# Kernel optimization log

Hardware: AMD Instinct MI355X
Metric: run time of the kernel (lower is better)

The kernel has to match this reference:

```python
import jax, jax.numpy as jnp
import numpy as np

HIDDEN = 2048
NUM_EXPERTS = 64
TOP_K = 2


def setup_inputs() -> dict:
    key = jax.random.key(0)
    k1, k2 = jax.random.split(key)
    x = jax.random.normal(k1, (4, 4096, HIDDEN), dtype=jnp.float32)
    # nn.Linear(hidden, num_experts, bias=False): weight shape [E, H], y = x @ W.T
    W = jax.random.normal(k2, (NUM_EXPERTS, HIDDEN), dtype=jnp.float32) * (HIDDEN ** -0.5)
    return {"x": x, "W": W}


def reference(x, W):
    B, S, H = x.shape
    E, K = NUM_EXPERTS, TOP_K
    xf = x.reshape(-1, H)                       # [N, H]
    gate_logits = xf @ W.T                      # [N, E]
    routing_probs = jax.nn.softmax(gate_logits, axis=-1)
    top_k_probs, top_k_indices = jax.lax.top_k(routing_probs, K)  # [N, K]
    denom = jnp.sum(top_k_probs, axis=-1, keepdims=True) + 1e-6
    routing_weights = (top_k_probs / denom).reshape(B, S, K)
    expert_indices = top_k_indices.reshape(B, S, K)

    # aux load-balancing loss (training path)
    N = xf.shape[0]
    # expert_mask.mean(0): fraction of tokens assigned to each expert
    assign_per_expert = jnp.zeros((E,), jnp.float32).at[top_k_indices.reshape(-1)].add(1.0) / N
    prob_per_expert = jnp.mean(routing_probs, axis=0)             # [E]
    aux_loss = (jnp.sum(prob_per_expert * prob_per_expert) * E
                + jnp.sum(assign_per_expert * assign_per_expert) * E)

    # expert_counts update (bincount over selected indices)
    expert_counts = jnp.zeros((E,), jnp.float32).at[top_k_indices.reshape(-1)].add(1.0)

    return routing_weights, expert_indices, aux_loss, expert_counts
```

## Files before the change

### kernel.cpp

```cpp
#include <hip/hip_runtime.h>

#define HID 2048
#define NEXP 64
#define NTOK 16384
#define TM 32
#define NTHREADS 256
#define NCHUNK 32
#define KPH 4
#define CPW 8
#define WS_W_OFF 1024
#define CHUNK_B 24576

#define OUT_IDX_OFF (2 * NTOK)
#define OUT_AUX_OFF (4 * NTOK)
#define OUT_CNT_OFF (4 * NTOK + 1)

typedef __attribute__((ext_vector_type(8))) short bhalf8;
typedef __attribute__((ext_vector_type(16))) float f32x16;

__device__ __forceinline__ void split3(float v, unsigned short& h1, unsigned short& h2, unsigned short& h3) {
    unsigned int u = __float_as_uint(v);
    unsigned int r1 = (u + 0x7FFFu + ((u >> 16) & 1u)) & 0xFFFF0000u;
    float f1 = __uint_as_float(r1);
    float d1 = v - f1;
    unsigned int u2 = __float_as_uint(d1);
    unsigned int r2 = (u2 + 0x7FFFu + ((u2 >> 16) & 1u)) & 0xFFFF0000u;
    float f2 = __uint_as_float(r2);
    float d2 = d1 - f2;
    h1 = (unsigned short)(r1 >> 16);
    h2 = (unsigned short)(r2 >> 16);
    h3 = (unsigned short)(__float_as_uint(d2) >> 16);
}

__device__ __forceinline__ void xsplit(float4 va, float4 vb, bhalf8& o1, bhalf8& o2, bhalf8& o3) {
    float f[8] = {va.x, va.y, va.z, va.w, vb.x, vb.y, vb.z, vb.w};
    union U { bhalf8 v; unsigned int u[4]; } u1, u2, u3;
#pragma unroll
    for (int t = 0; t < 4; t++) {
        float a = f[2 * t], b = f[2 * t + 1];
        unsigned int ua = __float_as_uint(a), ub = __float_as_uint(b);
        float da = a - __uint_as_float(ua & 0xFFFF0000u);
        float db = b - __uint_as_float(ub & 0xFFFF0000u);
        unsigned int uda = __float_as_uint(da), udb = __float_as_uint(db);
        float da2 = da - __uint_as_float(uda & 0xFFFF0000u);
        float db2 = db - __uint_as_float(udb & 0xFFFF0000u);
        u1.u[t] = (ua >> 16) | (ub & 0xFFFF0000u);
        u2.u[t] = (uda >> 16) | (udb & 0xFFFF0000u);
        u3.u[t] = (__float_as_uint(da2) >> 16) | (__float_as_uint(db2) & 0xFFFF0000u);
    }
    o1 = u1.v; o2 = u2.v; o3 = u3.v;
}

__global__ __launch_bounds__(256) void wsplit_kernel(const float* __restrict__ W,
                                                     char* __restrict__ wq,
                                                     float* __restrict__ wsf) {
    if (blockIdx.x == 0 && threadIdx.x < 2 * NEXP) wsf[threadIdx.x] = 0.f;
    int idx8 = (blockIdx.x * 256 + threadIdx.x) * 8;
    int e = idx8 >> 11;
    int k0 = idx8 & 2047;
    int c = k0 >> 6, ks = (k0 >> 4) & 3, half = (k0 >> 3) & 1;
    int g = e >> 5, l = (e & 31) + 32 * half;
    const float4* wp = (const float4*)(W + (size_t)e * HID + k0);
    float4 v0 = wp[0], v1 = wp[1];
    float f[8] = {v0.x, v0.y, v0.z, v0.w, v1.x, v1.y, v1.z, v1.w};
    unsigned int p1[4], p2[4], p3[4];
#pragma unroll
    for (int t = 0; t < 4; t++) {
        unsigned short a1, a2, a3, b1, b2, b3;
        split3(f[2 * t], a1, a2, a3);
        split3(f[2 * t + 1], b1, b2, b3);
        p1[t] = (unsigned int)a1 | ((unsigned int)b1 << 16);
        p2[t] = (unsigned int)a2 | ((unsigned int)b2 << 16);
        p3[t] = (unsigned int)a3 | ((unsigned int)b3 << 16);
    }
    char* base = wq + (size_t)(((c * 4 + ks) * 3 + 0) * 2 + g) * 1024 + l * 16;
    *(uint4*)(base)        = make_uint4(p1[0], p1[1], p1[2], p1[3]);
    *(uint4*)(base + 2048) = make_uint4(p2[0], p2[1], p2[2], p2[3]);
    *(uint4*)(base + 4096) = make_uint4(p3[0], p3[1], p3[2], p3[3]);
}

__global__ __launch_bounds__(NTHREADS, 2) void router_main(
    const float* __restrict__ x, const char* __restrict__ wq,
    float* __restrict__ out, float* __restrict__ ws_accum)
{
    __shared__ float slab[KPH * TM * 68];
    __shared__ float smax[TM];
    __shared__ float sinvZ[TM];
    __shared__ float scount[NEXP];

    const int tid = threadIdx.x;
    const int w = tid >> 6;
    const int lane = tid & 63;
    const int r = lane & 31;
    const int h = lane >> 5;
    const int n0 = blockIdx.x * TM;

    const float* xrow = x + (size_t)(n0 + r) * HID + h * 8;

    f32x16 acc0, acc1;
#pragma unroll
    for (int i = 0; i < 16; i++) { acc0[i] = 0.f; acc1[i] = 0.f; }

#pragma unroll 1
    for (int i = 0; i < CPW; ++i) {
        const int c = w * CPW + i;
        const float* xc = xrow + c * 64;
        float4 pxa[4], pxb[4];
#pragma unroll
        for (int ks = 0; ks < 4; ks++) {
            pxa[ks] = *(const float4*)(xc + ks * 16);
            pxb[ks] = *(const float4*)(xc + ks * 16 + 4);
        }
        const char* wc = wq + (size_t)c * CHUNK_B + lane * 16;
#pragma unroll
        for (int ks = 0; ks < 4; ks++) {
            bhalf8 A1, A2, A3;
            xsplit(pxa[ks], pxb[ks], A1, A2, A3);
            const char* wk = wc + ks * 6144;
            {
                bhalf8 B1 = *(const bhalf8*)(wk);
                bhalf8 B2 = *(const bhalf8*)(wk + 2048);
                bhalf8 B3 = *(const bhalf8*)(wk + 4096);
                acc0 = __builtin_amdgcn_mfma_f32_32x32x16_bf16(A1, B1, acc0, 0, 0, 0);
                acc0 = __builtin_amdgcn_mfma_f32_32x32x16_bf16(A1, B2, acc0, 0, 0, 0);
                acc0 = __builtin_amdgcn_mfma_f32_32x32x16_bf16(A2, B1, acc0, 0, 0, 0);
                acc0 = __builtin_amdgcn_mfma_f32_32x32x16_bf16(A1, B3, acc0, 0, 0, 0);
                acc0 = __builtin_amdgcn_mfma_f32_32x32x16_bf16(A2, B2, acc0, 0, 0, 0);
                acc0 = __builtin_amdgcn_mfma_f32_32x32x16_bf16(A3, B1, acc0, 0, 0, 0);
            }
            {
                bhalf8 B1 = *(const bhalf8*)(wk + 1024);
                bhalf8 B2 = *(const bhalf8*)(wk + 2048 + 1024);
                bhalf8 B3 = *(const bhalf8*)(wk + 4096 + 1024);
                acc1 = __builtin_amdgcn_mfma_f32_32x32x16_bf16(A1, B1, acc1, 0, 0, 0);
                acc1 = __builtin_amdgcn_mfma_f32_32x32x16_bf16(A1, B2, acc1, 0, 0, 0);
                acc1 = __builtin_amdgcn_mfma_f32_32x32x16_bf16(A2, B1, acc1, 0, 0, 0);
                acc1 = __builtin_amdgcn_mfma_f32_32x32x16_bf16(A1, B3, acc1, 0, 0, 0);
                acc1 = __builtin_amdgcn_mfma_f32_32x32x16_bf16(A2, B2, acc1, 0, 0, 0);
                acc1 = __builtin_amdgcn_mfma_f32_32x32x16_bf16(A3, B1, acc1, 0, 0, 0);
            }
        }
    }

#pragma unroll
    for (int reg = 0; reg < 16; reg++) {
        int row = (reg & 3) + 8 * (reg >> 2) + 4 * h;
        slab[(w * TM + row) * 68 + r]      = acc0[reg];
        slab[(w * TM + row) * 68 + 32 + r] = acc1[reg];
    }
    if (tid < NEXP) scount[tid] = 0.f;
    __syncthreads();

    float* logits = slab;
#pragma unroll
    for (int idx = tid; idx < TM * NEXP; idx += NTHREADS) {
        int t = idx >> 6, e = idx & 63;
        float v = slab[(0 * TM + t) * 68 + e] + slab[(1 * TM + t) * 68 + e]
                + slab[(2 * TM + t) * 68 + e] + slab[(3 * TM + t) * 68 + e];
        logits[t * 68 + e] = v;
    }
    __syncthreads();

    if (tid < TM) {
        const int t = tid;
        float m1 = -3.4e38f, m2 = -3.4e38f;
        int i1 = 0, i2 = 0;
        for (int e = 0; e < NEXP; e++) {
            float v = logits[t * 68 + e];
            if (v > m1) { m2 = m1; i2 = i1; m1 = v; i1 = e; }
            else if (v > m2) { m2 = v; i2 = e; }
        }
        float Z = 0.f;
        for (int e = 0; e < NEXP; e++)
            Z += __expf(logits[t * 68 + e] - m1);
        float invZ = 1.f / Z;
        float p1 = invZ;
        float p2 = __expf(m2 - m1) * invZ;
        float denom = p1 + p2 + 1e-6f;
        int n = n0 + t;
        out[2 * n + 0] = p1 / denom;
        out[2 * n + 1] = p2 / denom;
        out[OUT_IDX_OFF + 2 * n + 0] = (float)i1;
        out[OUT_IDX_OFF + 2 * n + 1] = (float)i2;
        smax[t] = m1;
        sinvZ[t] = invZ;
        atomicAdd(&scount[i1], 1.f);
        atomicAdd(&scount[i2], 1.f);
    }
    __syncthreads();

    if (tid < NEXP) {
        const int e = tid;
        float s = 0.f;
        for (int t = 0; t < TM; t++)
            s += __expf(logits[t * 68 + e] - smax[t]) * sinvZ[t];
        atomicAdd(&ws_accum[e], s);
        atomicAdd(&ws_accum[NEXP + e], scount[e]);
    }
}

__global__ void router_finish(const float* __restrict__ ws_accum,
                              float* __restrict__ out)
{
    const int e = threadIdx.x;
    const float invN = 1.f / (float)NTOK;
    float p = ws_accum[e] * invN;
    float a = ws_accum[NEXP + e] * invN;
    float v = p * p + a * a;
#pragma unroll
    for (int off = 32; off > 0; off >>= 1)
        v += __shfl_down(v, off);
    if (e == 0) out[OUT_AUX_OFF] = v * (float)NEXP;
    out[OUT_CNT_OFF + e] = ws_accum[NEXP + e];
}

extern "C" void kernel_launch(void* const* d_in, const int* in_sizes, int n_in,
                              void* d_out, int out_size, void* d_ws, size_t ws_size,
                              hipStream_t stream)
{
    const float* x = (const float*)d_in[0];
    const float* W = (const float*)d_in[1];
    float* out = (float*)d_out;
    float* wsf = (float*)d_ws;
    char* wq = (char*)d_ws + WS_W_OFF;

    wsplit_kernel<<<64, 256, 0, stream>>>(W, wq, wsf);
    router_main<<<NTOK / TM, NTHREADS, 0, stream>>>(x, wq, out, wsf);
    router_finish<<<1, 64, 0, stream>>>(wsf, out);
}
```

Baseline: 217.5 us.

## Double-buffer x chunk loads and replace global atomics with per-block partials

The main loop now prefetches the next x chunk into a second register set while computing the current chunk, so global load latency overlaps the MFMA work. Per-expert probability sums are computed by all 256 threads into shared memory instead of 64. Each block writes its partial sums to a workspace array rather than doing global atomics, and the finish kernel reduces the 512 partials serially. This removes global atomic contention and the zeroing step, but adds register pressure from the extra buffer and a serial 512-iteration reduction in a single-block finish kernel.

```diff
diff --git a/kernel.cpp b/kernel.cpp
--- a/kernel.cpp
+++ b/kernel.cpp
@@ -5,11 +5,12 @@
 #define NTOK 16384
 #define TM 32
 #define NTHREADS 256
+#define NBLK (NTOK / TM)
 #define NCHUNK 32
 #define KPH 4
 #define CPW 8
-#define WS_W_OFF 1024
 #define CHUNK_B 24576
+#define WS_W_OFF 262144
 
 #define OUT_IDX_OFF (2 * NTOK)
 #define OUT_AUX_OFF (4 * NTOK)
@@ -52,9 +53,7 @@
 }
 
 __global__ __launch_bounds__(256) void wsplit_kernel(const float* __restrict__ W,
-                                                     char* __restrict__ wq,
-                                                     float* __restrict__ wsf) {
-    if (blockIdx.x == 0 && threadIdx.x < 2 * NEXP) wsf[threadIdx.x] = 0.f;
+                                                     char* __restrict__ wq) {
     int idx8 = (blockIdx.x * 256 + threadIdx.x) * 8;
     int e = idx8 >> 11;
     int k0 = idx8 & 2047;
@@ -79,14 +78,51 @@
     *(uint4*)(base + 4096) = make_uint4(p3[0], p3[1], p3[2], p3[3]);
 }
 
+__device__ __forceinline__ void load_chunk(const float* xc, float4 (&pa)[4], float4 (&pb)[4]) {
+#pragma unroll
+    for (int ks = 0; ks < 4; ks++) {
+        pa[ks] = *(const float4*)(xc + ks * 16);
+        pb[ks] = *(const float4*)(xc + ks * 16 + 4);
+    }
+}
+
+__device__ __forceinline__ void compute_chunk(const float4 (&pa)[4], const float4 (&pb)[4],
+                                              const char* wc, f32x16& acc0, f32x16& acc1) {
+#pragma unroll
+    for (int ks = 0; ks < 4; ks++) {
+        bhalf8 A1, A2, A3;
+        xsplit(pa[ks], pb[ks], A1, A2, A3);
+        const char* wk = wc + ks * 6144;
+        bhalf8 B1 = *(const bhalf8*)(wk);
+        bhalf8 B2 = *(const bhalf8*)(wk + 2048);
+        bhalf8 B3 = *(const bhalf8*)(wk + 4096);
+        acc0 = __builtin_amdgcn_mfma_f32_32x32x16_bf16(A1, B1, acc0, 0, 0, 0);
+        acc0 = __builtin_amdgcn_mfma_f32_32x32x16_bf16(A1, B2, acc0, 0, 0, 0);
+        acc0 = __builtin_amdgcn_mfma_f32_32x32x16_bf16(A2, B1, acc0, 0, 0, 0);
+        acc0 = __builtin_amdgcn_mfma_f32_32x32x16_bf16(A1, B3, acc0, 0, 0, 0);
+        acc0 = __builtin_amdgcn_mfma_f32_32x32x16_bf16(A2, B2, acc0, 0, 0, 0);
+        acc0 = __builtin_amdgcn_mfma_f32_32x32x16_bf16(A3, B1, acc0, 0, 0, 0);
+        bhalf8 C1 = *(const bhalf8*)(wk + 1024);
+        bhalf8 C2 = *(const bhalf8*)(wk + 2048 + 1024);
+        bhalf8 C3 = *(const bhalf8*)(wk + 4096 + 1024);
+        acc1 = __builtin_amdgcn_mfma_f32_32x32x16_bf16(A1, C1, acc1, 0, 0, 0);
+        acc1 = __builtin_amdgcn_mfma_f32_32x32x16_bf16(A1, C2, acc1, 0, 0, 0);
+        acc1 = __builtin_amdgcn_mfma_f32_32x32x16_bf16(A2, C1, acc1, 0, 0, 0);
+        acc1 = __builtin_amdgcn_mfma_f32_32x32x16_bf16(A1, C3, acc1, 0, 0, 0);
+        acc1 = __builtin_amdgcn_mfma_f32_32x32x16_bf16(A2, C2, acc1, 0, 0, 0);
+        acc1 = __builtin_amdgcn_mfma_f32_32x32x16_bf16(A3, C1, acc1, 0, 0, 0);
+    }
+}
+
 __global__ __launch_bounds__(NTHREADS, 2) void router_main(
     const float* __restrict__ x, const char* __restrict__ wq,
-    float* __restrict__ out, float* __restrict__ ws_accum)
+    float* __restrict__ out, float* __restrict__ partials)
 {
     __shared__ float slab[KPH * TM * 68];
     __shared__ float smax[TM];
     __shared__ float sinvZ[TM];
     __shared__ float scount[NEXP];
+    __shared__ float sprob[NEXP];
 
     const int tid = threadIdx.x;
     const int w = tid >> 6;
@@ -101,45 +137,17 @@
 #pragma unroll
     for (int i = 0; i < 16; i++) { acc0[i] = 0.f; acc1[i] = 0.f; }
 
+    float4 pa0[4], pb0[4], pa1[4], pb1[4];
+    const float* xbase = xrow + (w * CPW) * 64;
+    load_chunk(xbase, pa0, pb0);
+    const char* wcbase = wq + (size_t)(w * CPW) * CHUNK_B + lane * 16;
+
 #pragma unroll 1
-    for (int i = 0; i < CPW; ++i) {
-        const int c = w * CPW + i;
-        const float* xc = xrow + c * 64;
-        float4 pxa[4], pxb[4];
-#pragma unroll
-        for (int ks = 0; ks < 4; ks++) {
-            pxa[ks] = *(const float4*)(xc + ks * 16);
-            pxb[ks] = *(const float4*)(xc + ks * 16 + 4);
-        }
-        const char* wc = wq + (size_t)c * CHUNK_B + lane * 16;
-#pragma unroll
-        for (int ks = 0; ks < 4; ks++) {
-            bhalf8 A1, A2, A3;
-            xsplit(pxa[ks], pxb[ks], A1, A2, A3);
-            const char* wk = wc + ks * 6144;
-            {
-                bhalf8 B1 = *(const bhalf8*)(wk);
-                bhalf8 B2 = *(const bhalf8*)(wk + 2048);
-                bhalf8 B3 = *(const bhalf8*)(wk + 4096);
-                acc0 = __builtin_amdgcn_mfma_f32_32x32x16_bf16(A1, B1, acc0, 0, 0, 0);
-                acc0 = __builtin_amdgcn_mfma_f32_32x32x16_bf16(A1, B2, acc0, 0, 0, 0);
-                acc0 = __builtin_amdgcn_mfma_f32_32x32x16_bf16(A2, B1, acc0, 0, 0, 0);
-                acc0 = __builtin_amdgcn_mfma_f32_32x32x16_bf16(A1, B3, acc0, 0, 0, 0);
-                acc0 = __builtin_amdgcn_mfma_f32_32x32x16_bf16(A2, B2, acc0, 0, 0, 0);
-                acc0 = __builtin_amdgcn_mfma_f32_32x32x16_bf16(A3, B1, acc0, 0, 0, 0);
-            }
-            {
-                bhalf8 B1 = *(const bhalf8*)(wk + 1024);
-                bhalf8 B2 = *(const bhalf8*)(wk + 2048 + 1024);
-                bhalf8 B3 = *(const bhalf8*)(wk + 4096 + 1024);
-                acc1 = __builtin_amdgcn_mfma_f32_32x32x16_bf16(A1, B1, acc1, 0, 0, 0);
-                acc1 = __builtin_amdgcn_mfma_f32_32x32x16_bf16(A1, B2, acc1, 0, 0, 0);
-                acc1 = __builtin_amdgcn_mfma_f32_32x32x16_bf16(A2, B1, acc1, 0, 0, 0);
-                acc1 = __builtin_amdgcn_mfma_f32_32x32x16_bf16(A1, B3, acc1, 0, 0, 0);
-                acc1 = __builtin_amdgcn_mfma_f32_32x32x16_bf16(A2, B2, acc1, 0, 0, 0);
-                acc1 = __builtin_amdgcn_mfma_f32_32x32x16_bf16(A3, B1, acc1, 0, 0, 0);
-            }
-        }
+    for (int i = 0; i < CPW; i += 2) {
+        if (i + 1 < CPW) load_chunk(xbase + (i + 1) * 64, pa1, pb1);
+        compute_chunk(pa0, pb0, wcbase + (size_t)i * CHUNK_B, acc0, acc1);
+        if (i + 2 < CPW) load_chunk(xbase + (i + 2) * 64, pa0, pb0);
+        if (i + 1 < CPW) compute_chunk(pa1, pb1, wcbase + (size_t)(i + 1) * CHUNK_B, acc0, acc1);
     }
 
 #pragma unroll
@@ -148,16 +156,15 @@
         slab[(w * TM + row) * 68 + r]      = acc0[reg];
         slab[(w * TM + row) * 68 + 32 + r] = acc1[reg];
     }
-    if (tid < NEXP) scount[tid] = 0.f;
+    if (tid < NEXP) { scount[tid] = 0.f; sprob[tid] = 0.f; }
     __syncthreads();
 
     float* logits = slab;
 #pragma unroll
     for (int idx = tid; idx < TM * NEXP; idx += NTHREADS) {
         int t = idx >> 6, e = idx & 63;
-        float v = slab[(0 * TM + t) * 68 + e] + slab[(1 * TM + t) * 68 + e]
-                + slab[(2 * TM + t) * 68 + e] + slab[(3 * TM + t) * 68 + e];
-        logits[t * 68 + e] = v;
+        logits[t * 68 + e] = slab[(0 * TM + t) * 68 + e] + slab[(1 * TM + t) * 68 + e]
+                           + slab[(2 * TM + t) * 68 + e] + slab[(3 * TM + t) * 68 + e];
     }
     __syncthreads();
 
@@ -189,29 +196,43 @@
     }
     __syncthreads();
 
+    {
+        const int e = tid & 63, tq = tid >> 6;
+        float s = 0.f;
+#pragma unroll
+        for (int j = 0; j < 8; j++) {
+            int t = tq * 8 + j;
+            s += __expf(logits[t * 68 + e] - smax[t]) * sinvZ[t];
+        }
+        atomicAdd(&sprob[e], s);
+    }
+    __syncthreads();
+
     if (tid < NEXP) {
-        const int e = tid;
-        float s = 0.f;
-        for (int t = 0; t < TM; t++)
-            s += __expf(logits[t * 68 + e] - smax[t]) * sinvZ[t];
-        atomicAdd(&ws_accum[e], s);
-        atomicAdd(&ws_accum[NEXP + e], scount[e]);
-    }
-}
-
-__global__ void router_finish(const float* __restrict__ ws_accum,
-                              float* __restrict__ out)
+        partials[blockIdx.x * 128 + tid]      = sprob[tid];
+        partials[blockIdx.x * 128 + 64 + tid] = scount[tid];
+    }
+}
+
+__global__ __launch_bounds__(128) void router_finish(const float* __restrict__ partials,
+                                                     float* __restrict__ out)
 {
-    const int e = threadIdx.x;
+    __shared__ float red[2];
+    const int t = threadIdx.x;
+    float s = 0.f;
+#pragma unroll 8
+    for (int b = 0; b < NBLK; b++)
+        s += partials[b * 128 + t];
     const float invN = 1.f / (float)NTOK;
-    float p = ws_accum[e] * invN;
-    float a = ws_accum[NEXP + e] * invN;
-    float v = p * p + a * a;
+    if (t >= 64) out[OUT_CNT_OFF + (t - 64)] = s;
+    float sc = s * invN;
+    float v = sc * sc;
 #pragma unroll
     for (int off = 32; off > 0; off >>= 1)
         v += __shfl_down(v, off);
-    if (e == 0) out[OUT_AUX_OFF] = v * (float)NEXP;
-    out[OUT_CNT_OFF + e] = ws_accum[NEXP + e];
+    if ((t & 63) == 0) red[t >> 6] = v;
+    __syncthreads();
+    if (t == 0) out[OUT_AUX_OFF] = (red[0] + red[1]) * (float)NEXP;
 }
 
 extern "C" void kernel_launch(void* const* d_in, const int* in_sizes, int n_in,
@@ -221,10 +242,10 @@
     const float* x = (const float*)d_in[0];
     const float* W = (const float*)d_in[1];
     float* out = (float*)d_out;
-    float* wsf = (float*)d_ws;
+    float* partials = (float*)d_ws;
     char* wq = (char*)d_ws + WS_W_OFF;
 
-    wsplit_kernel<<<64, 256, 0, stream>>>(W, wq, wsf);
-    router_main<<<NTOK / TM, NTHREADS, 0, stream>>>(x, wq, out, wsf);
-    router_finish<<<1, 64, 0, stream>>>(wsf, out);
-}
+    wsplit_kernel<<<64, 256, 0, stream>>>(W, wq);
+    router_main<<<NBLK, NTHREADS, 0, stream>>>(x, wq, out, partials);
+    router_finish<<<1, 128, 0, stream>>>(partials, out);
+}
```

New measurement: 229.9 us. 1.06x slower.
